# Kernel optimization log

Hardware: AMD Instinct MI355X
Metric: run time of the kernel (lower is better)

The kernel has to match this reference:

```python
import jax, jax.numpy as jnp
import numpy as np

N, E = 10000, 320000
F_N, F_E, F_G, LATENT, F_OUT = 128, 128, 32, 128, 128


def _make_mlp_params(key, dims):
    # dims: list of layer widths, e.g. [256,128,128,128,256]
    params = []
    for i in range(len(dims) - 1):
        key, k1, k2 = jax.random.split(key, 3)
        lim = 1.0 / np.sqrt(dims[i])
        w = jax.random.uniform(k1, (dims[i], dims[i + 1]), jnp.float32, -lim, lim)
        b = jax.random.uniform(k2, (dims[i + 1],), jnp.float32, -lim, lim)
        params.append((w, b))
    return params, key


def _mlp(h, ws, bs, activate_final):
    n = len(ws)
    for i in range(n):
        h = h @ ws[i] + bs[i]
        if i < n - 1 or activate_final:
            h = jax.nn.relu(h)
    return h


def setup_inputs() -> dict:
    key = jax.random.key(0)
    key, kx, ke, kg, ki = jax.random.split(key, 5)
    x = jax.random.normal(kx, (N, F_N), jnp.float32)
    edge_index = jax.random.randint(ki, (2, E), 0, N, jnp.int64)
    edge_attr = jax.random.normal(ke, (E, F_E), jnp.float32)
    global_attr = jax.random.normal(kg, (1, F_G), jnp.float32)

    # node_mlp_1: (F_N+F_E) -> L -> L -> L -> (F_N+F_E), activate_final=True
    p1, key = _make_mlp_params(key, [F_N + F_E, LATENT, LATENT, LATENT, F_N + F_E])
    # node_mlp_2: (2*F_N+F_E+F_G) -> L -> L -> L -> F_OUT, activate_final=False
    p2, key = _make_mlp_params(key, [2 * F_N + F_E + F_G, LATENT, LATENT, LATENT, F_OUT])

    inp = {"x": x, "edge_index": edge_index, "edge_attr": edge_attr, "global_attr": global_attr}
    for i, (w, b) in enumerate(p1):
        inp[f"m1_w{i}"] = w
        inp[f"m1_b{i}"] = b
    for i, (w, b) in enumerate(p2):
        inp[f"m2_w{i}"] = w
        inp[f"m2_b{i}"] = b
    return inp


def reference(x, edge_index, edge_attr, global_attr,
              m1_w0, m1_b0, m1_w1, m1_b1, m1_w2, m1_b2, m1_w3, m1_b3,
              m2_w0, m2_b0, m2_w1, m2_b1, m2_w2, m2_b2, m2_w3, m2_b3):
    row, col = edge_index[0], edge_index[1]
    n = x.shape[0]
    # gather sender-side node feats, per-edge MLP (activate_final=True)
    h = jnp.concatenate([x[row], edge_attr], axis=1)          # [E, F_N+F_E]
    h = _mlp(h, [m1_w0, m1_w1, m1_w2, m1_w3], [m1_b0, m1_b1, m1_b2, m1_b3], True)
    # scatter_mean over destination nodes
    s = jax.ops.segment_sum(h, col, num_segments=n)           # [N, F_N+F_E]
    cnt = jax.ops.segment_sum(jnp.ones((h.shape[0],), h.dtype), col, num_segments=n)
    agg = s / jnp.maximum(cnt, 1.0)[:, None]
    # repeat global feats to N rows (pad_to_size mode='repeat', G divides N)
    g = jnp.tile(global_attr, (n // global_attr.shape[0], 1))  # [N, F_G]
    out = jnp.concatenate([x, agg, g], axis=1)                 # [N, 2F_N+F_E+F_G]
    return _mlp(out, [m2_w0, m2_w1, m2_w2, m2_w3], [m2_b0, m2_b1, m2_b2, m2_b3], False)
```

## Files before the change

kernel.cpp:

```cpp
#include <hip/hip_runtime.h>
#include <hip/hip_bf16.h>

#define E_EDGES 320000
#define N_NODES 10000

typedef __attribute__((ext_vector_type(8))) short short8;
typedef __attribute__((ext_vector_type(4))) float floatx4;

__device__ __forceinline__ float bf2f(unsigned short u) {
    union { unsigned int i; float f; } v; v.i = ((unsigned int)u) << 16; return v.f;
}
__device__ __forceinline__ unsigned int pk2(float a, float b) {
    float2 t; t.x = a; t.y = b;
    __hip_bfloat162 h = __float22bfloat162_rn(t);
    union { __hip_bfloat162 h; unsigned int u; } c; c.h = h; return c.u;
}

template<int K, int Nn, int FT, int ET>
__device__ __forceinline__ void layer_acc(const unsigned short* __restrict__ in, int istride,
                                          const unsigned short* __restrict__ wt,
                                          int lane, int n0, floatx4 (&acc)[FT][ET])
{
    const int quad = lane >> 4;
    const int mrow = lane & 15;
    floatx4 zero = {0.f, 0.f, 0.f, 0.f};
#pragma unroll
    for (int ft = 0; ft < FT; ++ft)
#pragma unroll
        for (int et = 0; et < ET; ++et)
            acc[ft][et] = zero;

#pragma unroll
    for (int kt = 0; kt < K / 32; ++kt) {
        const int koff = kt * 32 + quad * 8;
        short8 a[FT];
        short8 b[ET];
#pragma unroll
        for (int ft = 0; ft < FT; ++ft)
            a[ft] = *(const short8*)&wt[(size_t)(kt * (Nn >> 4) + (n0 >> 4) + ft) * 512 + lane * 8];
#pragma unroll
        for (int et = 0; et < ET; ++et)
            b[et] = *(const short8*)&in[(et * 16 + mrow) * istride + koff];
#pragma unroll
        for (int ft = 0; ft < FT; ++ft)
#pragma unroll
            for (int et = 0; et < ET; ++et)
                acc[ft][et] = __builtin_amdgcn_mfma_f32_16x16x32_bf16(a[ft], b[et], acc[ft][et], 0, 0, 0);
    }
}

template<int FT, int ET>
__device__ __forceinline__ void store_lds(floatx4 (&acc)[FT][ET], const float* __restrict__ bias,
                                          int lane, int n0, unsigned short* __restrict__ out, int ostride,
                                          bool relu)
{
    const int quad = lane >> 4, mrow = lane & 15;
#pragma unroll
    for (int ft = 0; ft < FT; ++ft) {
        int fbase = n0 + ft * 16 + quad * 4;
        float4 bv = *(const float4*)&bias[fbase];
#pragma unroll
        for (int et = 0; et < ET; ++et) {
            int edge = et * 16 + mrow;
            float v0 = acc[ft][et][0] + bv.x;
            float v1 = acc[ft][et][1] + bv.y;
            float v2 = acc[ft][et][2] + bv.z;
            float v3 = acc[ft][et][3] + bv.w;
            if (relu) {
                v0 = v0 > 0.f ? v0 : 0.f; v1 = v1 > 0.f ? v1 : 0.f;
                v2 = v2 > 0.f ? v2 : 0.f; v3 = v3 > 0.f ? v3 : 0.f;
            }
            uint2 pk; pk.x = pk2(v0, v1); pk.y = pk2(v2, v3);
            *(uint2*)&out[edge * ostride + fbase] = pk;
        }
    }
}

struct TDesc { const float* src; unsigned short* dst; int nElem; int logN; int blockStart; };
struct TArgs { TDesc d[8]; };

__global__ void prep_kernel(TArgs a, const int* __restrict__ eidx, int* __restrict__ cnt, int histStart)
{
    int b = blockIdx.x;
    if (b >= histStart) {
        int e = (b - histStart) * 256 + threadIdx.x;
        if (e < E_EDGES) atomicAdd(&cnt[eidx[E_EDGES + e]], 1);
        return;
    }
    int i = 0;
#pragma unroll
    for (int j = 1; j < 8; ++j)
        if (b >= a.d[j].blockStart) i = j;
    const TDesc t = a.d[i];
    int idx = (b - t.blockStart) * 256 + threadIdx.x;
    if (idx < t.nElem) {
        int n = idx & ((1 << t.logN) - 1);
        int k = idx >> t.logN;
        int ntiles = 1 << (t.logN - 4);
        size_t dsti = ((size_t)(k >> 5) * ntiles + (n >> 4)) * 512
                    + ((k >> 3) & 3) * 128 + (n & 15) * 8 + (k & 7);
        union { float f; unsigned int u; } c; c.f = t.src[idx];
        unsigned int uu = c.u;
        t.dst[dsti] = (unsigned short)((uu + 0x7fffu + ((uu >> 16) & 1u)) >> 16);
    }
}

__global__ void scan_kernel(const int* __restrict__ cnt, int* __restrict__ fill)
{
    __shared__ int partial[256];
    const int CH = 40;
    int tid = threadIdx.x;
    int base = tid * CH;
    int local[CH];
    int sum = 0;
#pragma unroll
    for (int j = 0; j < CH; ++j) {
        int idx = base + j;
        int c = (idx < N_NODES) ? cnt[idx] : 0;
        local[j] = c;
        sum += c;
    }
    partial[tid] = sum;
    __syncthreads();
    for (int o = 1; o < 256; o <<= 1) {
        int v = (tid >= o) ? partial[tid - o] : 0;
        __syncthreads();
        partial[tid] += v;
        __syncthreads();
    }
    int run = partial[tid] - sum;
#pragma unroll
    for (int j = 0; j < CH; ++j) {
        int idx = base + j;
        if (idx < N_NODES) fill[idx] = run;
        run += local[j];
    }
}

__global__ void fill_kernel(const int* __restrict__ eidx, int* __restrict__ fill,
                            int4* __restrict__ epack)
{
    int e = blockIdx.x * 256 + threadIdx.x;
    int c = eidx[E_EDGES + e];
    int r = eidx[e];
    int pos = atomicAdd(&fill[c], 1);
    int4 rec; rec.x = e; rec.y = r; rec.z = c; rec.w = 0;
    epack[pos] = rec;
}

__global__ __launch_bounds__(256, 3) void edge_kernel(
    const float* __restrict__ x,
    const float* __restrict__ ea,
    const int4* __restrict__ epack,
    const unsigned short* __restrict__ wt0, const float* __restrict__ b0,
    const unsigned short* __restrict__ wt1, const float* __restrict__ b1,
    const unsigned short* __restrict__ wt2, const float* __restrict__ b2,
    const unsigned short* __restrict__ wt3, const float* __restrict__ b3,
    float* __restrict__ s)
{
    __shared__ __align__(16) char U[51200];
    __shared__ int dsw[4][64];

    unsigned short* H0 = (unsigned short*)U;
    unsigned short* H1 = (unsigned short*)(U + 33792);
    unsigned short* H2 = (unsigned short*)U;
    unsigned short* H3 = H1;
    unsigned short* G  = (unsigned short*)U;

    const int tid = threadIdx.x;
    const int lane = tid & 63;
    const int wave = __builtin_amdgcn_readfirstlane(tid >> 6);
    const int p0 = blockIdx.x * 64;

    dsw[wave][lane] = epack[p0 + lane].z;

#pragma unroll
    for (int i = 0; i < 16; ++i) {
        int row = wave + i * 4;
        int e = epack[p0 + row].x;
        int r = epack[p0 + row].y;
        float4 v;
        if (lane < 32) v = *(const float4*)(x + (size_t)r * 128 + lane * 4);
        else           v = *(const float4*)(ea + (size_t)e * 128 + (lane - 32) * 4);
        uint2 pk; pk.x = pk2(v.x, v.y); pk.y = pk2(v.z, v.w);
        *(uint2*)&H0[row * 264 + lane * 4] = pk;
    }
    __syncthreads();

    {
        floatx4 acc[2][4];
        layer_acc<256, 128, 2, 4>(H0, 264, wt0, lane, wave * 32, acc);
        store_lds<2, 4>(acc, b0, lane, wave * 32, H1, 136, true);
    }
    __syncthreads();
    {
        floatx4 acc[2][4];
        layer_acc<128, 128, 2, 4>(H1, 136, wt1, lane, wave * 32, acc);
        store_lds<2, 4>(acc, b1, lane, wave * 32, H2, 136, true);
    }
    __syncthreads();
    {
        floatx4 acc[2][4];
        layer_acc<128, 128, 2, 4>(H2, 136, wt2, lane, wave * 32, acc);
        store_lds<2, 4>(acc, b2, lane, wave * 32, H3, 136, true);
    }
    __syncthreads();
    {
        floatx4 acc[4][4];
        layer_acc<128, 256, 4, 4>(H3, 136, wt3, lane, wave * 64, acc);
        store_lds<4, 4>(acc, b3, lane, wave * 64, G, 264, true);
    }

    {
        int cp = lane & 31;
        int half = lane >> 5;
        int col2 = wave * 64 + cp * 2;
        int base = half * 32;
        const int* dsl = dsw[wave];
        float s0 = 0.f, s1 = 0.f;
#pragma unroll 4
        for (int i = 0; i < 32; ++i) {
            int gi = base + i;
            unsigned int u = *(const unsigned int*)&G[gi * 264 + col2];
            s0 += bf2f((unsigned short)u);
            s1 += bf2f((unsigned short)(u >> 16));
            if (i == 31 || dsl[gi + 1] != dsl[gi]) {
                float* dst = &s[(size_t)dsl[gi] * 256 + col2];
                atomicAdd(dst, s0);
                atomicAdd(dst + 1, s1);
                s0 = 0.f; s1 = 0.f;
            }
        }
    }
}

__global__ __launch_bounds__(256, 2) void node_kernel(
    const float* __restrict__ x,
    const float* __restrict__ g,
    const float* __restrict__ s,
    const int* __restrict__ cnt,
    const unsigned short* __restrict__ wt0, const float* __restrict__ b0,
    const unsigned short* __restrict__ wt1, const float* __restrict__ b1,
    const unsigned short* __restrict__ wt2, const float* __restrict__ b2,
    const unsigned short* __restrict__ wt3, const float* __restrict__ b3,
    float* __restrict__ out)
{
    __shared__ __align__(16) char NU[71680];
    unsigned short* Abig = (unsigned short*)NU;
    unsigned short* HsA  = (unsigned short*)(NU + 54272);
    unsigned short* HsB  = (unsigned short*)NU;

    const int tid = threadIdx.x;
    const int node0 = blockIdx.x * 64;

#pragma unroll
    for (int i = 0; i < 8; ++i) {
        int task = tid + i * 256;
        int row = task >> 5, part = task & 31;
        int node = node0 + row;
        uint2 pk = {0u, 0u};
        if (node < N_NODES) {
            float4 v = *(const float4*)(x + (size_t)node * 128 + part * 4);
            pk.x = pk2(v.x, v.y); pk.y = pk2(v.z, v.w);
        }
        *(uint2*)&Abig[row * 424 + part * 4] = pk;
    }
#pragma unroll
    for (int i = 0; i < 16; ++i) {
        int task = tid + i * 256;
        int row = task >> 6, part = task & 63;
        int node = node0 + row;
        uint2 pk = {0u, 0u};
        if (node < N_NODES) {
            float c = (float)cnt[node];
            float inv = 1.f / (c > 1.f ? c : 1.f);
            floatx4 v = *(const floatx4*)(s + (size_t)node * 256 + part * 4);
            pk.x = pk2(v[0] * inv, v[1] * inv);
            pk.y = pk2(v[2] * inv, v[3] * inv);
        }
        *(uint2*)&Abig[row * 424 + 128 + part * 4] = pk;
    }
#pragma unroll
    for (int i = 0; i < 2; ++i) {
        int task = tid + i * 256;
        int row = task >> 3, part = task & 7;
        float4 v = *(const float4*)(g + part * 4);
        uint2 pk; pk.x = pk2(v.x, v.y); pk.y = pk2(v.z, v.w);
        *(uint2*)&Abig[row * 424 + 384 + part * 4] = pk;
    }
    __syncthreads();

    const int lane = tid & 63;
    const int wave = tid >> 6;

    {
        floatx4 acc[2][4];
        layer_acc<416, 128, 2, 4>(Abig, 424, wt0, lane, wave * 32, acc);
        store_lds<2, 4>(acc, b0, lane, wave * 32, HsA, 136, true);
    }
    __syncthreads();
    {
        floatx4 acc[2][4];
        layer_acc<128, 128, 2, 4>(HsA, 136, wt1, lane, wave * 32, acc);
        store_lds<2, 4>(acc, b1, lane, wave * 32, HsB, 136, true);
    }
    __syncthreads();
    {
        floatx4 acc[2][4];
        layer_acc<128, 128, 2, 4>(HsB, 136, wt2, lane, wave * 32, acc);
        store_lds<2, 4>(acc, b2, lane, wave * 32, HsA, 136, true);
    }
    __syncthreads();
    {
        floatx4 acc[2][4];
        layer_acc<128, 128, 2, 4>(HsA, 136, wt3, lane, wave * 32, acc);
        const int quad = lane >> 4, mrow = lane & 15;
#pragma unroll
        for (int ft = 0; ft < 2; ++ft) {
            int fbase = wave * 32 + ft * 16 + quad * 4;
            float4 bv = *(const float4*)&b3[fbase];
#pragma unroll
            for (int et = 0; et < 4; ++et) {
                int node = node0 + et * 16 + mrow;
                if (node < N_NODES) {
                    float4 o;
                    o.x = acc[ft][et][0] + bv.x;
                    o.y = acc[ft][et][1] + bv.y;
                    o.z = acc[ft][et][2] + bv.z;
                    o.w = acc[ft][et][3] + bv.w;
                    *(float4*)&out[(size_t)node * 128 + fbase] = o;
                }
            }
        }
    }
}

extern "C" void kernel_launch(void* const* d_in, const int* in_sizes, int n_in,
                              void* d_out, int out_size, void* d_ws, size_t ws_size,
                              hipStream_t stream)
{
    (void)in_sizes; (void)n_in; (void)out_size; (void)ws_size;

    const float* x  = (const float*)d_in[0];
    const int* eidx = (const int*)d_in[1];
    const float* ea = (const float*)d_in[2];
    const float* g  = (const float*)d_in[3];

    const float* w1[4]  = { (const float*)d_in[4],  (const float*)d_in[6],
                            (const float*)d_in[8],  (const float*)d_in[10] };
    const float* bb1[4] = { (const float*)d_in[5],  (const float*)d_in[7],
                            (const float*)d_in[9],  (const float*)d_in[11] };
    const float* w2[4]  = { (const float*)d_in[12], (const float*)d_in[14],
                            (const float*)d_in[16], (const float*)d_in[18] };
    const float* bb2[4] = { (const float*)d_in[13], (const float*)d_in[15],
                            (const float*)d_in[17], (const float*)d_in[19] };

    char* p = (char*)d_ws;
    unsigned short* wt1_0 = (unsigned short*)p; p += 256 * 128 * 2;
    unsigned short* wt1_1 = (unsigned short*)p; p += 128 * 128 * 2;
    unsigned short* wt1_2 = (unsigned short*)p; p += 128 * 128 * 2;
    unsigned short* wt1_3 = (unsigned short*)p; p += 128 * 256 * 2;
    unsigned short* wt2_0 = (unsigned short*)p; p += 416 * 128 * 2;
    unsigned short* wt2_1 = (unsigned short*)p; p += 128 * 128 * 2;
    unsigned short* wt2_2 = (unsigned short*)p; p += 128 * 128 * 2;
    unsigned short* wt2_3 = (unsigned short*)p; p += 128 * 128 * 2;
    float* s    = (float*)p; p += (size_t)N_NODES * 256 * 4;
    int* cnt    = (int*)p;   p += (size_t)N_NODES * 4;
    int* fill   = (int*)p;   p += (size_t)N_NODES * 4;
    int4* epack = (int4*)p;  p += (size_t)E_EDGES * 16;

    hipMemsetAsync(s, 0, (size_t)N_NODES * 256 * 4 + (size_t)N_NODES * 4, stream);

    TArgs ta;
    int bs = 0;
    auto set = [&](int i, const float* src, unsigned short* dst, int K, int Nn, int logN) {
        ta.d[i].src = src; ta.d[i].dst = dst; ta.d[i].nElem = K * Nn;
        ta.d[i].logN = logN; ta.d[i].blockStart = bs;
        bs += (K * Nn + 255) / 256;
    };
    set(0, w1[0], wt1_0, 256, 128, 7);
    set(1, w1[1], wt1_1, 128, 128, 7);
    set(2, w1[2], wt1_2, 128, 128, 7);
    set(3, w1[3], wt1_3, 128, 256, 8);
    set(4, w2[0], wt2_0, 416, 128, 7);
    set(5, w2[1], wt2_1, 128, 128, 7);
    set(6, w2[2], wt2_2, 128, 128, 7);
    set(7, w2[3], wt2_3, 128, 128, 7);

    int histBlocks = E_EDGES / 256;
    hipLaunchKernelGGL(prep_kernel, dim3(bs + histBlocks), dim3(256), 0, stream,
                       ta, eidx, cnt, bs);
    hipLaunchKernelGGL(scan_kernel, dim3(1), dim3(256), 0, stream, cnt, fill);
    hipLaunchKernelGGL(fill_kernel, dim3(E_EDGES / 256), dim3(256), 0, stream,
                       eidx, fill, epack);

    hipLaunchKernelGGL(edge_kernel, dim3(E_EDGES / 64), dim3(256), 0, stream,
                       x, ea, epack,
                       wt1_0, bb1[0], wt1_1, bb1[1], wt1_2, bb1[2], wt1_3, bb1[3],
                       s);

    hipLaunchKernelGGL(node_kernel, dim3((N_NODES + 63) / 64), dim3(256), 0, stream,
                       x, g, s, cnt,
                       wt2_0, bb2[0], wt2_1, bb2[1], wt2_2, bb2[2], wt2_3, bb2[3],
                       (float*)d_out);
}
```

Baseline: 476.8 us.

## Shrink edge and node MLP tiles to 32 rows with two-wave blocks

Edge and node kernels now handle 32 rows per block with 128 threads, where each wave covers 64 output features across two 16-row MFMA tiles. Previously a block handled 64 rows with 4 waves of 32 features each. Edge metadata is staged once into shared arrays, and the scatter loop now walks all 32 rows per wave-column. The smaller LDS footprint and blocks are meant to raise occupancy and improve load balance. In exchange, weight reuse per block is halved, so weight traffic from L2 roughly doubles and more atomic flushes happen at block boundaries.

```diff
diff --git a/kernel.cpp b/kernel.cpp
--- a/kernel.cpp
+++ b/kernel.cpp
@@ -61,7 +61,7 @@
         float4 bv = *(const float4*)&bias[fbase];
 #pragma unroll
         for (int et = 0; et < ET; ++et) {
-            int edge = et * 16 + mrow;
+            int row = et * 16 + mrow;
             float v0 = acc[ft][et][0] + bv.x;
             float v1 = acc[ft][et][1] + bv.y;
             float v2 = acc[ft][et][2] + bv.z;
@@ -71,7 +71,7 @@
                 v2 = v2 > 0.f ? v2 : 0.f; v3 = v3 > 0.f ? v3 : 0.f;
             }
             uint2 pk; pk.x = pk2(v0, v1); pk.y = pk2(v2, v3);
-            *(uint2*)&out[edge * ostride + fbase] = pk;
+            *(uint2*)&out[row * ostride + fbase] = pk;
         }
     }
 }
@@ -148,7 +148,7 @@
     epack[pos] = rec;
 }
 
-__global__ __launch_bounds__(256, 3) void edge_kernel(
+__global__ __launch_bounds__(128, 3) void edge_kernel(
     const float* __restrict__ x,
     const float* __restrict__ ea,
     const int4* __restrict__ epack,
@@ -158,74 +158,72 @@
     const unsigned short* __restrict__ wt3, const float* __restrict__ b3,
     float* __restrict__ s)
 {
-    __shared__ __align__(16) char U[51200];
-    __shared__ int dsw[4][64];
+    __shared__ __align__(16) char U[25600];
+    __shared__ int es[32], rs[32], ds[32];
 
     unsigned short* H0 = (unsigned short*)U;
-    unsigned short* H1 = (unsigned short*)(U + 33792);
+    unsigned short* H1 = (unsigned short*)(U + 16896);
     unsigned short* H2 = (unsigned short*)U;
     unsigned short* H3 = H1;
     unsigned short* G  = (unsigned short*)U;
 
     const int tid = threadIdx.x;
     const int lane = tid & 63;
-    const int wave = __builtin_amdgcn_readfirstlane(tid >> 6);
-    const int p0 = blockIdx.x * 64;
-
-    dsw[wave][lane] = epack[p0 + lane].z;
+    const int wave = tid >> 6;
+    const int p0 = blockIdx.x * 32;
+
+    if (tid < 32) {
+        int4 rec = epack[p0 + tid];
+        es[tid] = rec.x; rs[tid] = rec.y; ds[tid] = rec.z;
+    }
+    __syncthreads();
 
 #pragma unroll
     for (int i = 0; i < 16; ++i) {
-        int row = wave + i * 4;
-        int e = epack[p0 + row].x;
-        int r = epack[p0 + row].y;
+        int task = tid + i * 128;
+        int row = task >> 6, part = task & 63;
         float4 v;
-        if (lane < 32) v = *(const float4*)(x + (size_t)r * 128 + lane * 4);
-        else           v = *(const float4*)(ea + (size_t)e * 128 + (lane - 32) * 4);
+        if (part < 32) v = *(const float4*)(x + (size_t)rs[row] * 128 + part * 4);
+        else           v = *(const float4*)(ea + (size_t)es[row] * 128 + (part - 32) * 4);
         uint2 pk; pk.x = pk2(v.x, v.y); pk.y = pk2(v.z, v.w);
-        *(uint2*)&H0[row * 264 + lane * 4] = pk;
-    }
-    __syncthreads();
-
-    {
-        floatx4 acc[2][4];
-        layer_acc<256, 128, 2, 4>(H0, 264, wt0, lane, wave * 32, acc);
-        store_lds<2, 4>(acc, b0, lane, wave * 32, H1, 136, true);
-    }
-    __syncthreads();
-    {
-        floatx4 acc[2][4];
-        layer_acc<128, 128, 2, 4>(H1, 136, wt1, lane, wave * 32, acc);
-        store_lds<2, 4>(acc, b1, lane, wave * 32, H2, 136, true);
-    }
-    __syncthreads();
-    {
-        floatx4 acc[2][4];
-        layer_acc<128, 128, 2, 4>(H2, 136, wt2, lane, wave * 32, acc);
-        store_lds<2, 4>(acc, b2, lane, wave * 32, H3, 136, true);
-    }
-    __syncthreads();
-    {
-        floatx4 acc[4][4];
-        layer_acc<128, 256, 4, 4>(H3, 136, wt3, lane, wave * 64, acc);
-        store_lds<4, 4>(acc, b3, lane, wave * 64, G, 264, true);
-    }
-
-    {
-        int cp = lane & 31;
-        int half = lane >> 5;
-        int col2 = wave * 64 + cp * 2;
-        int base = half * 32;
-        const int* dsl = dsw[wave];
+        *(uint2*)&H0[row * 264 + part * 4] = pk;
+    }
+    __syncthreads();
+
+    {
+        floatx4 acc[4][2];
+        layer_acc<256, 128, 4, 2>(H0, 264, wt0, lane, wave * 64, acc);
+        store_lds<4, 2>(acc, b0, lane, wave * 64, H1, 136, true);
+    }
+    __syncthreads();
+    {
+        floatx4 acc[4][2];
+        layer_acc<128, 128, 4, 2>(H1, 136, wt1, lane, wave * 64, acc);
+        store_lds<4, 2>(acc, b1, lane, wave * 64, H2, 136, true);
+    }
+    __syncthreads();
+    {
+        floatx4 acc[4][2];
+        layer_acc<128, 128, 4, 2>(H2, 136, wt2, lane, wave * 64, acc);
+        store_lds<4, 2>(acc, b2, lane, wave * 64, H3, 136, true);
+    }
+    __syncthreads();
+    {
+        floatx4 acc[8][2];
+        layer_acc<128, 256, 8, 2>(H3, 136, wt3, lane, wave * 128, acc);
+        store_lds<8, 2>(acc, b3, lane, wave * 128, G, 264, true);
+    }
+
+    {
+        int col2 = wave * 128 + lane * 2;
         float s0 = 0.f, s1 = 0.f;
 #pragma unroll 4
         for (int i = 0; i < 32; ++i) {
-            int gi = base + i;
-            unsigned int u = *(const unsigned int*)&G[gi * 264 + col2];
+            unsigned int u = *(const unsigned int*)&G[i * 264 + col2];
             s0 += bf2f((unsigned short)u);
             s1 += bf2f((unsigned short)(u >> 16));
-            if (i == 31 || dsl[gi + 1] != dsl[gi]) {
-                float* dst = &s[(size_t)dsl[gi] * 256 + col2];
+            if (i == 31 || ds[i + 1] != ds[i]) {
+                float* dst = &s[(size_t)ds[i] * 256 + col2];
                 atomicAdd(dst, s0);
                 atomicAdd(dst + 1, s1);
                 s0 = 0.f; s1 = 0.f;
@@ -234,7 +232,7 @@
     }
 }
 
-__global__ __launch_bounds__(256, 2) void node_kernel(
+__global__ __launch_bounds__(128, 2) void node_kernel(
     const float* __restrict__ x,
     const float* __restrict__ g,
     const float* __restrict__ s,
@@ -245,17 +243,19 @@
     const unsigned short* __restrict__ wt3, const float* __restrict__ b3,
     float* __restrict__ out)
 {
-    __shared__ __align__(16) char NU[71680];
+    __shared__ __align__(16) char NU[35840];
     unsigned short* Abig = (unsigned short*)NU;
-    unsigned short* HsA  = (unsigned short*)(NU + 54272);
+    unsigned short* HsA  = (unsigned short*)(NU + 27136);
     unsigned short* HsB  = (unsigned short*)NU;
 
     const int tid = threadIdx.x;
-    const int node0 = blockIdx.x * 64;
+    const int lane = tid & 63;
+    const int wave = tid >> 6;
+    const int node0 = blockIdx.x * 32;
 
 #pragma unroll
     for (int i = 0; i < 8; ++i) {
-        int task = tid + i * 256;
+        int task = tid + i * 128;
         int row = task >> 5, part = task & 31;
         int node = node0 + row;
         uint2 pk = {0u, 0u};
@@ -267,7 +267,7 @@
     }
 #pragma unroll
     for (int i = 0; i < 16; ++i) {
-        int task = tid + i * 256;
+        int task = tid + i * 128;
         int row = task >> 6, part = task & 63;
         int node = node0 + row;
         uint2 pk = {0u, 0u};
@@ -282,7 +282,7 @@
     }
 #pragma unroll
     for (int i = 0; i < 2; ++i) {
-        int task = tid + i * 256;
+        int task = tid + i * 128;
         int row = task >> 3, part = task & 7;
         float4 v = *(const float4*)(g + part * 4);
         uint2 pk; pk.x = pk2(v.x, v.y); pk.y = pk2(v.z, v.w);
@@ -290,37 +290,34 @@
     }
     __syncthreads();
 
-    const int lane = tid & 63;
-    const int wave = tid >> 6;
-
-    {
-        floatx4 acc[2][4];
-        layer_acc<416, 128, 2, 4>(Abig, 424, wt0, lane, wave * 32, acc);
-        store_lds<2, 4>(acc, b0, lane, wave * 32, HsA, 136, true);
-    }
-    __syncthreads();
-    {
-        floatx4 acc[2][4];
-        layer_acc<128, 128, 2, 4>(HsA, 136, wt1, lane, wave * 32, acc);
-        store_lds<2, 4>(acc, b1, lane, wave * 32, HsB, 136, true);
-    }
-    __syncthreads();
-    {
-        floatx4 acc[2][4];
-        layer_acc<128, 128, 2, 4>(HsB, 136, wt2, lane, wave * 32, acc);
-        store_lds<2, 4>(acc, b2, lane, wave * 32, HsA, 136, true);
-    }
-    __syncthreads();
-    {
-        floatx4 acc[2][4];
-        layer_acc<128, 128, 2, 4>(HsA, 136, wt3, lane, wave * 32, acc);
+    {
+        floatx4 acc[4][2];
+        layer_acc<416, 128, 4, 2>(Abig, 424, wt0, lane, wave * 64, acc);
+        store_lds<4, 2>(acc, b0, lane, wave * 64, HsA, 136, true);
+    }
+    __syncthreads();
+    {
+        floatx4 acc[4][2];
+        layer_acc<128, 128, 4, 2>(HsA, 136, wt1, lane, wave * 64, acc);
+        store_lds<4, 2>(acc, b1, lane, wave * 64, HsB, 136, true);
+    }
+    __syncthreads();
+    {
+        floatx4 acc[4][2];
+        layer_acc<128, 128, 4, 2>(HsB, 136, wt2, lane, wave * 64, acc);
+        store_lds<4, 2>(acc, b2, lane, wave * 64, HsA, 136, true);
+    }
+    __syncthreads();
+    {
+        floatx4 acc[4][2];
+        layer_acc<128, 128, 4, 2>(HsA, 136, wt3, lane, wave * 64, acc);
         const int quad = lane >> 4, mrow = lane & 15;
 #pragma unroll
-        for (int ft = 0; ft < 2; ++ft) {
-            int fbase = wave * 32 + ft * 16 + quad * 4;
+        for (int ft = 0; ft < 4; ++ft) {
+            int fbase = wave * 64 + ft * 16 + quad * 4;
             float4 bv = *(const float4*)&b3[fbase];
 #pragma unroll
-            for (int et = 0; et < 4; ++et) {
+            for (int et = 0; et < 2; ++et) {
                 int node = node0 + et * 16 + mrow;
                 if (node < N_NODES) {
                     float4 o;
@@ -394,12 +391,12 @@
     hipLaunchKernelGGL(fill_kernel, dim3(E_EDGES / 256), dim3(256), 0, stream,
                        eidx, fill, epack);
 
-    hipLaunchKernelGGL(edge_kernel, dim3(E_EDGES / 64), dim3(256), 0, stream,
+    hipLaunchKernelGGL(edge_kernel, dim3(E_EDGES / 32), dim3(128), 0, stream,
                        x, ea, epack,
                        wt1_0, bb1[0], wt1_1, bb1[1], wt1_2, bb1[2], wt1_3, bb1[3],
                        s);
 
-    hipLaunchKernelGGL(node_kernel, dim3((N_NODES + 63) / 64), dim3(256), 0, stream,
+    hipLaunchKernelGGL(node_kernel, dim3((N_NODES + 31) / 32), dim3(128), 0, stream,
                        x, g, s, cnt,
                        wt2_0, bb2[0], wt2_1, bb2[1], wt2_2, bb2[2], wt2_3, bb2[3],
                        (float*)d_out);
```

Result: slower. 490.9 us (+3.0%).
